# Kernel tuning notes

Hardware: AMD Instinct MI355X
Metric: run time of the kernel (lower is better)

The kernel has to match this reference:

```python
import jax, jax.numpy as jnp
import numpy as np

B, C, L = 8, 512, 4096
KC, VC, H = 512, 512, 8
DK, DV = KC // H, VC // H
EPS = 1e-5


def _ln(x, g, b):
    m = jnp.mean(x, axis=-1, keepdims=True)
    v = jnp.var(x, axis=-1, keepdims=True)
    return (x - m) * jax.lax.rsqrt(v + EPS) * g + b


def setup_inputs() -> dict:
    key = jax.random.key(0)
    ks = jax.random.split(key, 12)
    s = 0.02
    return {
        "z1": jax.random.normal(ks[0], (B, C, L), jnp.float32),
        "z2": jax.random.normal(ks[1], (B, C, L), jnp.float32),
        "Wq": jax.random.normal(ks[2], (KC, C), jnp.float32) * s,
        "bq": jnp.zeros((KC,), jnp.float32),
        "Wk": jax.random.normal(ks[3], (KC, C), jnp.float32) * s,
        "bk": jnp.zeros((KC,), jnp.float32),
        "Wv": jax.random.normal(ks[4], (VC, C), jnp.float32) * s,
        "bv": jnp.zeros((VC,), jnp.float32),
        "Wr": jax.random.normal(ks[5], (C, VC), jnp.float32) * s,
        "br": jnp.zeros((C,), jnp.float32),
        "g1": jnp.ones((C,), jnp.float32),
        "be1": jnp.zeros((C,), jnp.float32),
        "W1": jax.random.normal(ks[6], (2 * C, C), jnp.float32) * s,
        "b1": jnp.zeros((2 * C,), jnp.float32),
        "W2": jax.random.normal(ks[7], (C, 2 * C), jnp.float32) * s,
        "b2": jnp.zeros((C,), jnp.float32),
        "g2": jnp.ones((C,), jnp.float32),
        "be2": jnp.zeros((C,), jnp.float32),
    }


def reference(z1, z2, Wq, bq, Wk, bk, Wv, bv, Wr, br, g1, be1, W1, b1, W2, b2, g2, be2):
    # 1x1 Conv1d projections (channels-first)
    q = jnp.einsum('oc,bcl->bol', Wq, z1) + bq[None, :, None]
    k = jnp.einsum('oc,bcl->bol', Wk, z2) + bk[None, :, None]
    v = jnp.einsum('oc,bcl->bol', Wv, z2) + bv[None, :, None]
    qh = q.reshape(B, H, DK, L)
    kh = k.reshape(B, H, DK, L)
    vh = v.reshape(B, H, DV, L)
    # efficient attention: keys softmax over length, queries over channels
    kh = jax.nn.softmax(kh, axis=-1)
    qh = jax.nn.softmax(qh, axis=2)
    ctx = jnp.einsum('bhkl,bhvl->bhkv', kh, vh)          # [B,H,DK,DV]
    att = jnp.einsum('bhkv,bhkl->bhvl', ctx, qh)          # [B,H,DV,L]
    att = att.reshape(B, VC, L)
    z = jnp.einsum('oc,bcl->bol', Wr, att) + br[None, :, None] + z1  # reprojection + residual
    # b c l -> b l c, LayerNorm, FFN, back
    x = z.transpose(0, 2, 1)
    x = _ln(x, g1, be1)
    h = jax.nn.elu(x @ W1.T + b1)
    y = h @ W2.T + b2
    y = _ln(y, g2, be2)
    return y.transpose(0, 2, 1)
```

## Files before the change

kernel.cpp:

```cpp
#include <hip/hip_runtime.h>
#include <math.h>

#define B_   8
#define C_   512
#define L_   4096
#define H_   8
#define DK_  64
#define C2_  1024

typedef unsigned short ushort;
typedef short     bf16x8_t __attribute__((ext_vector_type(8)));
typedef float     f32x4_t  __attribute__((ext_vector_type(4)));
typedef unsigned short u16x8 __attribute__((ext_vector_type(8)));
typedef unsigned short u16x4 __attribute__((ext_vector_type(4)));

__device__ __forceinline__ float bf2f(ushort u) {
    unsigned int x = ((unsigned int)u) << 16;
    float f; __builtin_memcpy(&f, &x, 4); return f;
}
__device__ __forceinline__ ushort f2bf(float f) {
    unsigned int x; __builtin_memcpy(&x, &f, 4);
    x = (x + 0x7FFFu + ((x >> 16) & 1u)) >> 16;
    return (ushort)x;
}

#define GLOAD_LDS16(gp, lp) \
    __builtin_amdgcn_global_load_lds((const __attribute__((address_space(1))) void*)(gp), \
                                     (__attribute__((address_space(3))) void*)(lp), 16, 0, 0)

__global__ __launch_bounds__(256) void transpose_in(const float* __restrict__ in,
                                                    ushort* __restrict__ out)
{
    const int b = blockIdx.z, c0 = blockIdx.y * 64, l0 = blockIdx.x * 64;
    __shared__ float t[64][65];
    const int tid = threadIdx.x;
    {
        const int c = tid >> 4, l4 = (tid & 15) * 4;
        const float* ip = in + ((size_t)b * C_ + c0) * L_ + l0;
#pragma unroll
        for (int cc = c; cc < 64; cc += 16) {
            float4 v = *(const float4*)(ip + (size_t)cc * L_ + l4);
            t[l4 + 0][cc] = v.x; t[l4 + 1][cc] = v.y;
            t[l4 + 2][cc] = v.z; t[l4 + 3][cc] = v.w;
        }
    }
    __syncthreads();
    {
        const int l = tid >> 3, c8 = (tid & 7) * 8;
        ushort* op = out + ((size_t)b * L_ + l0) * C_ + c0;
#pragma unroll
        for (int ll = l; ll < 64; ll += 32) {
            u16x8 v;
#pragma unroll
            for (int i = 0; i < 8; ++i) v[i] = f2bf(t[ll][c8 + i]);
            *(u16x8*)(op + (size_t)ll * C_ + c8) = v;
        }
    }
}

__global__ __launch_bounds__(256) void transpose_out(const float* __restrict__ in,
                                                     float* __restrict__ out)
{
    const int b = blockIdx.z, c0 = blockIdx.y * 64, l0 = blockIdx.x * 64;
    __shared__ float t[64][65];
    const int tid = threadIdx.x;
    {
        const int l = tid >> 4, c4 = (tid & 15) * 4;
#pragma unroll
        for (int ll = l; ll < 64; ll += 16) {
            float4 v = *(const float4*)(in + ((size_t)(b * L_ + l0 + ll)) * C_ + c0 + c4);
            t[c4 + 0][ll] = v.x; t[c4 + 1][ll] = v.y;
            t[c4 + 2][ll] = v.z; t[c4 + 3][ll] = v.w;
        }
    }
    __syncthreads();
    {
        const int c = tid >> 4, l4 = (tid & 15) * 4;
        float* op = out + ((size_t)b * C_ + c0) * L_ + l0;
#pragma unroll
        for (int cc = c; cc < 64; cc += 16) {
            float4 v = {t[cc][l4], t[cc][l4 + 1], t[cc][l4 + 2], t[cc][l4 + 3]};
            *(float4*)(op + (size_t)cc * L_ + l4) = v;
        }
    }
}

__global__ __launch_bounds__(256) void cvt_bf16(const float* __restrict__ in,
                                                ushort* __restrict__ out, int n4)
{
    const int i = blockIdx.x * 256 + threadIdx.x;
    if (i < n4) {
        float4 v = *(const float4*)(in + 4 * (size_t)i);
        u16x4 o; o[0] = f2bf(v.x); o[1] = f2bf(v.y); o[2] = f2bf(v.z); o[3] = f2bf(v.w);
        *(u16x4*)(out + 4 * (size_t)i) = o;
    }
}

__global__ __launch_bounds__(256) void zero_kernel(float* __restrict__ p, int n4)
{
    const int i = blockIdx.x * 256 + threadIdx.x;
    if (i < n4) { float4 z = {0.f, 0.f, 0.f, 0.f}; *(float4*)(p + 4 * (size_t)i) = z; }
}

template<int ACT, bool HAS_RES>
__global__ __launch_bounds__(512, 2) void conv_mfma(
    const ushort* __restrict__ A, const ushort* __restrict__ Wt,
    const float* __restrict__ bias, const ushort* __restrict__ res,
    ushort* __restrict__ out, int M, int N, int K)
{
    const int m0 = blockIdx.x * 256;
    const int n0 = blockIdx.y * 256;
    const int tid = threadIdx.x;
    const int w = tid >> 6, lane = tid & 63;
    const int wm2 = (w >> 2) * 128, wn = (w & 3) * 64;
    const int l16 = lane & 15, quad = lane >> 4;

    __shared__ ushort smem[65536];

    const int sRow = tid >> 1, sHalf = tid & 1;
    const int sh = sHalf ^ ((sRow >> 2) & 1);
    const ushort* gA = A  + (size_t)(m0 + sRow) * K + sh * 8;
    const ushort* gB = Wt + (size_t)(n0 + sRow) * K + sh * 8;
    const int ldst = tid * 8;

    const int baseA = wm2 + l16;
    const int baseB = wn + l16;
    const int hA = (quad & 1) ^ ((baseA >> 2) & 1);
    const int hB = (quad & 1) ^ ((baseB >> 2) & 1);
    const int qhi = (quad >> 1) * 4096;
    const int aoff = qhi + baseA * 16 + hA * 8;
    const int boff = qhi + 16384 + baseB * 16 + hB * 8;

    f32x4_t acc[8][4];
#pragma unroll
    for (int i = 0; i < 8; ++i)
#pragma unroll
        for (int j = 0; j < 4; ++j) acc[i][j] = (f32x4_t){0.f, 0.f, 0.f, 0.f};

    const int nt = K >> 6;

#pragma unroll
    for (int q = 0; q < 4; ++q) {
        GLOAD_LDS16(gA + q * 16, smem + q * 4096 + ldst);
        GLOAD_LDS16(gB + q * 16, smem + 16384 + q * 4096 + ldst);
    }

    for (int t = 0; t < nt; ++t) {
        const int cb = (t & 1) * 32768;
        const int nb = 32768 - cb;
        const bool pf = (t + 1 < nt);
#pragma unroll
        for (int p = 0; p < 4; ++p) {
            if (pf) {
                const int ko = (t + 1) * 64 + p * 16;
                GLOAD_LDS16(gA + ko, smem + nb + p * 4096 + ldst);
                GLOAD_LDS16(gB + ko, smem + nb + 16384 + p * 4096 + ldst);
                asm volatile("s_waitcnt vmcnt(6)" ::: "memory");
            } else {
                if (p < 2) { asm volatile("s_waitcnt vmcnt(4)" ::: "memory"); }
                else       { asm volatile("s_waitcnt vmcnt(0)" ::: "memory"); }
            }
            __builtin_amdgcn_s_barrier();
            asm volatile("" ::: "memory");

            const int ih = p & 1;
            const ushort* base = smem + cb + (p >> 1) * 8192;
            bf16x8_t wf[4], af[4];
#pragma unroll
            for (int x = 0; x < 4; ++x) {
                wf[x] = *(const bf16x8_t*)(base + boff + x * 256);
                af[x] = *(const bf16x8_t*)(base + aoff + (ih * 4 + x) * 256);
            }
            __builtin_amdgcn_s_setprio(1);
#pragma unroll
            for (int x = 0; x < 4; ++x)
#pragma unroll
                for (int j = 0; j < 4; ++j)
                    acc[ih * 4 + x][j] =
                        __builtin_amdgcn_mfma_f32_16x16x32_bf16(wf[j], af[x], acc[ih * 4 + x][j], 0, 0, 0);
            __builtin_amdgcn_s_setprio(0);
        }
    }

    __syncthreads();
    ushort* sT = smem + w * 4608;
#pragma unroll
    for (int h2 = 0; h2 < 2; ++h2) {
#pragma unroll
        for (int j = 0; j < 4; ++j) {
            const int nb4 = wn + j * 16 + quad * 4;
            const float4 bo = *(const float4*)(bias + n0 + nb4);
            const float bv[4] = {bo.x, bo.y, bo.z, bo.w};
#pragma unroll
            for (int x = 0; x < 4; ++x) {
                const int ml = x * 16 + l16;
                const int m = m0 + wm2 + h2 * 64 + ml;
                float v[4];
#pragma unroll
                for (int r = 0; r < 4; ++r) v[r] = acc[h2 * 4 + x][j][r] + bv[r];
                if (HAS_RES) {
                    const u16x4 rv = *(const u16x4*)(res + (size_t)m * N + n0 + nb4);
#pragma unroll
                    for (int r = 0; r < 4; ++r) v[r] += bf2f(rv[r]);
                }
                if (ACT == 1) {
#pragma unroll
                    for (int r = 0; r < 4; ++r) v[r] = (v[r] > 0.f) ? v[r] : (__expf(v[r]) - 1.f);
                }
                u16x4 pv;
#pragma unroll
                for (int r = 0; r < 4; ++r) pv[r] = f2bf(v[r]);
                *(u16x4*)(sT + ml * 72 + (nb4 - wn)) = pv;
            }
        }
        {
            const int rr = lane >> 3, ch = lane & 7;
#pragma unroll
            for (int rep = 0; rep < 8; ++rep) {
                const int ml = rep * 8 + rr;
                const u16x8 vo = *(const u16x8*)(sT + ml * 72 + ch * 8);
                *(u16x8*)(out + (size_t)(m0 + wm2 + h2 * 64 + ml) * N + n0 + wn + ch * 8) = vo;
            }
        }
    }
}

__global__ __launch_bounds__(256) void kstat_chunk(const ushort* __restrict__ k,
                                                   float2* __restrict__ stats)
{
    const int cg = blockIdx.x;
    const int bc = blockIdx.y;
    const int b = bc >> 3, ch = bc & 7;
    const int tid = threadIdx.x;
    const int g = tid & 7;
    const int kk = tid >> 3;
    const int w = tid >> 6, lane = tid & 63;
    const ushort* base = k + ((size_t)(b * L_) + ch * 512) * C_ + cg * 64 + g * 8;

    __shared__ float red[4][8][8];
    __shared__ float mcol[64];

    float fm[8];
#pragma unroll
    for (int i = 0; i < 8; ++i) fm[i] = -3.0e38f;
    for (int r = kk; r < 512; r += 32) {
        u16x8 v = *(const u16x8*)(base + (size_t)r * C_);
#pragma unroll
        for (int i = 0; i < 8; ++i) fm[i] = fmaxf(fm[i], bf2f(v[i]));
    }
#pragma unroll
    for (int off = 8; off <= 32; off <<= 1)
#pragma unroll
        for (int i = 0; i < 8; ++i) fm[i] = fmaxf(fm[i], __shfl_xor(fm[i], off));
    if ((lane >> 3) == 0)
#pragma unroll
        for (int i = 0; i < 8; ++i) red[w][g][i] = fm[i];
    __syncthreads();
    if (tid < 64) {
        const int g2 = tid >> 3, j = tid & 7;
        mcol[g2 * 8 + j] = fmaxf(fmaxf(red[0][g2][j], red[1][g2][j]),
                                 fmaxf(red[2][g2][j], red[3][g2][j]));
    }
    __syncthreads();
    float fmc[8];
#pragma unroll
    for (int i = 0; i < 8; ++i) fmc[i] = mcol[g * 8 + i];

    float fs[8] = {};
    for (int r = kk; r < 512; r += 32) {
        u16x8 v = *(const u16x8*)(base + (size_t)r * C_);
#pragma unroll
        for (int i = 0; i < 8; ++i) fs[i] += __expf(bf2f(v[i]) - fmc[i]);
    }
#pragma unroll
    for (int off = 8; off <= 32; off <<= 1)
#pragma unroll
        for (int i = 0; i < 8; ++i) fs[i] += __shfl_xor(fs[i], off);
    __syncthreads();
    if ((lane >> 3) == 0)
#pragma unroll
        for (int i = 0; i < 8; ++i) red[w][g][i] = fs[i];
    __syncthreads();
    if (tid < 64) {
        const int g2 = tid >> 3, j = tid & 7;
        const float s = red[0][g2][j] + red[1][g2][j] + red[2][g2][j] + red[3][g2][j];
        const int c = cg * 64 + g2 * 8 + j;
        stats[((size_t)(b * C_ + c)) * 8 + ch] = make_float2(mcol[g2 * 8 + j], s);
    }
}

__global__ __launch_bounds__(256) void kstat_merge(const float2* __restrict__ stats,
                                                   float2* __restrict__ minv)
{
    const int i = blockIdx.x * 256 + threadIdx.x;
    if (i >= B_ * C_) return;
    float2 st[8];
    float m = -3.0e38f;
#pragma unroll
    for (int ch = 0; ch < 8; ++ch) { st[ch] = stats[(size_t)i * 8 + ch]; m = fmaxf(m, st[ch].x); }
    float s = 0.f;
#pragma unroll
    for (int ch = 0; ch < 8; ++ch) s += st[ch].y * __expf(st[ch].x - m);
    minv[i] = make_float2(m, 1.f / s);
}

__global__ __launch_bounds__(256) void ctx_mfma(
    const ushort* __restrict__ kk, const ushort* __restrict__ vv,
    const float2* __restrict__ minv, float* __restrict__ ctx)
{
    const int bh = blockIdx.y, b = bh >> 3, h = bh & 7;
    const int l0 = blockIdx.x * 256;
    const int tid = threadIdx.x, w = tid >> 6, lane = tid & 63;
    const int l16 = lane & 15, quad = lane >> 4;

    __shared__ ushort sK[64 * 72];
    __shared__ ushort sV[64 * 72];

    const int grp = tid >> 7;
    const int st  = tid & 127;
    const int sc8 = (st & 7) * 8;
    const int sl4 = (st >> 3) * 4;
    const ushort* gsrc = (grp ? vv : kk)
        + ((size_t)(b * L_ + l0 + sl4)) * C_ + h * 64 + sc8;
    ushort* dst = grp ? sV : sK;

    float2 cst[8];
#pragma unroll
    for (int i = 0; i < 8; ++i)
        cst[i] = minv[(size_t)b * C_ + h * 64 + sc8 + i];

    f32x4_t acc[4];
#pragma unroll
    for (int j = 0; j < 4; ++j) acc[j] = (f32x4_t){0.f, 0.f, 0.f, 0.f};

    for (int tile = 0; tile < 4; ++tile) {
        u16x8 vr[4];
#pragma unroll
        for (int j = 0; j < 4; ++j)
            vr[j] = *(const u16x8*)(gsrc + ((size_t)(tile * 64 + j)) * C_);
        __syncthreads();
        if (grp == 0) {
#pragma unroll
            for (int c = 0; c < 8; ++c) {
                u16x4 o;
#pragma unroll
                for (int j = 0; j < 4; ++j)
                    o[j] = f2bf(__expf(bf2f(vr[j][c]) - cst[c].x) * cst[c].y);
                *(u16x4*)(dst + (sc8 + c) * 72 + sl4) = o;
            }
        } else {
#pragma unroll
            for (int c = 0; c < 8; ++c) {
                u16x4 o;
#pragma unroll
                for (int j = 0; j < 4; ++j) o[j] = vr[j][c];
                *(u16x4*)(dst + (sc8 + c) * 72 + sl4) = o;
            }
        }
        __syncthreads();
#pragma unroll
        for (int k0 = 0; k0 < 64; k0 += 32) {
            const bf16x8_t vf = *(const bf16x8_t*)(sV + (w * 16 + l16) * 72 + k0 + quad * 8);
#pragma unroll
            for (int j = 0; j < 4; ++j) {
                const bf16x8_t kf = *(const bf16x8_t*)(sK + (j * 16 + l16) * 72 + k0 + quad * 8);
                acc[j] = __builtin_amdgcn_mfma_f32_16x16x32_bf16(vf, kf, acc[j], 0, 0, 0);
            }
        }
    }
    float* cp = ctx + (size_t)bh * 4096;
#pragma unroll
    for (int j = 0; j < 4; ++j)
#pragma unroll
        for (int r = 0; r < 4; ++r)
            atomicAdd(&cp[(w * 16 + quad * 4 + r) * 64 + (j * 16 + l16)], acc[j][r]);
}

__global__ __launch_bounds__(256) void att_mfma(
    const ushort* __restrict__ q, const float* __restrict__ ctx,
    ushort* __restrict__ att)
{
    const int bh = blockIdx.y, b = bh >> 3, h = bh & 7;
    const int l0 = blockIdx.x * 128;
    const int tid = threadIdx.x, w = tid >> 6, lane = tid & 63;
    const int l16 = lane & 15, quad = lane >> 4;

    __shared__ ushort sQ[128 * 72];
    __shared__ ushort sC[64 * 72];

    {
        const int part = tid & 7;
#pragma unroll
        for (int rr = tid >> 3; rr < 128; rr += 32) {
            u16x8 v = *(const u16x8*)(q + ((size_t)(b * L_ + l0 + rr)) * C_ + h * 64 + part * 8);
            float f[8], m = -3.0e38f;
#pragma unroll
            for (int i = 0; i < 8; ++i) { f[i] = bf2f(v[i]); m = fmaxf(m, f[i]); }
            m = fmaxf(m, __shfl_xor(m, 1));
            m = fmaxf(m, __shfl_xor(m, 2));
            m = fmaxf(m, __shfl_xor(m, 4));
            float s = 0.f;
#pragma unroll
            for (int i = 0; i < 8; ++i) { f[i] = __expf(f[i] - m); s += f[i]; }
            s += __shfl_xor(s, 1); s += __shfl_xor(s, 2); s += __shfl_xor(s, 4);
            const float inv = 1.f / s;
            u16x8 o;
#pragma unroll
            for (int i = 0; i < 8; ++i) o[i] = f2bf(f[i] * inv);
            *(u16x8*)(sQ + rr * 72 + part * 8) = o;
        }
        const int dv = tid >> 2, dk0 = (tid & 3) * 16;
        const float* cp = ctx + (size_t)bh * 4096 + dv * 64 + dk0;
#pragma unroll
        for (int i = 0; i < 16; ++i) sC[dv * 72 + dk0 + i] = f2bf(cp[i]);
    }
    __syncthreads();

    f32x4_t acc[2][4];
#pragma unroll
    for (int i = 0; i < 2; ++i)
#pragma unroll
        for (int j = 0; j < 4; ++j) acc[i][j] = (f32x4_t){0.f, 0.f, 0.f, 0.f};

#pragma unroll
    for (int ks = 0; ks < 2; ++ks) {
        const int k0 = ks * 32;
        bf16x8_t aq[2], bc[4];
#pragma unroll
        for (int i = 0; i < 2; ++i)
            aq[i] = *(const bf16x8_t*)(sQ + (w * 32 + i * 16 + l16) * 72 + k0 + quad * 8);
#pragma unroll
        for (int j = 0; j < 4; ++j)
            bc[j] = *(const bf16x8_t*)(sC + (j * 16 + l16) * 72 + k0 + quad * 8);
#pragma unroll
        for (int i = 0; i < 2; ++i)
#pragma unroll
            for (int j = 0; j < 4; ++j)
                acc[i][j] = __builtin_amdgcn_mfma_f32_16x16x32_bf16(aq[i], bc[j], acc[i][j], 0, 0, 0);
    }

#pragma unroll
    for (int j = 0; j < 4; ++j)
#pragma unroll
        for (int i = 0; i < 2; ++i) {
            const int mb = l0 + w * 32 + i * 16 + quad * 4;
#pragma unroll
            for (int r = 0; r < 4; ++r)
                att[((size_t)(b * L_ + mb + r)) * C_ + h * 64 + j * 16 + l16] = f2bf(acc[i][j][r]);
        }
}

template<bool OUTF32>
__global__ __launch_bounds__(256) void ln_row(
    const ushort* __restrict__ in, const float* __restrict__ g,
    const float* __restrict__ be, ushort* __restrict__ outb,
    float* __restrict__ outf)
{
    const int tid = threadIdx.x, w = tid >> 6, lane = tid & 63;
    const size_t row = (size_t)blockIdx.x * 4 + w;
    const ushort* p = in + row * C_ + lane * 8;
    u16x8 v = *(const u16x8*)p;
    float f[8], s = 0.f, s2 = 0.f;
#pragma unroll
    for (int i = 0; i < 8; ++i) { f[i] = bf2f(v[i]); s += f[i]; s2 = fmaf(f[i], f[i], s2); }
#pragma unroll
    for (int o = 1; o < 64; o <<= 1) { s += __shfl_xor(s, o); s2 += __shfl_xor(s2, o); }
    const float mean = s * (1.f / C_);
    const float var  = s2 * (1.f / C_) - mean * mean;
    const float inv  = rsqrtf(var + 1e-5f);
    if (OUTF32) {
        float* op = outf + row * C_ + lane * 8;
#pragma unroll
        for (int i = 0; i < 8; ++i)
            op[i] = (f[i] - mean) * inv * g[lane * 8 + i] + be[lane * 8 + i];
    } else {
        u16x8 ov;
#pragma unroll
        for (int i = 0; i < 8; ++i)
            ov[i] = f2bf((f[i] - mean) * inv * g[lane * 8 + i] + be[lane * 8 + i]);
        *(u16x8*)(outb + row * C_ + lane * 8) = ov;
    }
}

extern "C" void kernel_launch(void* const* d_in, const int* in_sizes, int n_in,
                              void* d_out, int out_size, void* d_ws, size_t ws_size,
                              hipStream_t stream)
{
    const float* z1  = (const float*)d_in[0];
    const float* z2  = (const float*)d_in[1];
    const float* Wq  = (const float*)d_in[2];
    const float* bq  = (const float*)d_in[3];
    const float* Wk  = (const float*)d_in[4];
    const float* bk  = (const float*)d_in[5];
    const float* Wv  = (const float*)d_in[6];
    const float* bv  = (const float*)d_in[7];
    const float* Wr  = (const float*)d_in[8];
    const float* br  = (const float*)d_in[9];
    const float* g1  = (const float*)d_in[10];
    const float* be1 = (const float*)d_in[11];
    const float* W1  = (const float*)d_in[12];
    const float* b1  = (const float*)d_in[13];
    const float* W2  = (const float*)d_in[14];
    const float* b2  = (const float*)d_in[15];
    const float* g2  = (const float*)d_in[16];
    const float* be2 = (const float*)d_in[17];
    float* out = (float*)d_out;

    const size_t SB = (size_t)B_ * L_ * C_;
    ushort* ws16 = (ushort*)d_ws;
    ushort* b0v = ws16;
    ushort* b1v = ws16 + SB;
    ushort* b2v = ws16 + 2 * SB;
    ushort* b3v = ws16 + 3 * SB;
    ushort* wb  = ws16 + 4 * SB;
    ushort* wbq = wb;
    ushort* wbk = wb + 262144;
    ushort* wbv = wb + 524288;
    ushort* wbr = wb + 786432;
    ushort* wb1 = wb + 1048576;
    ushort* wb2 = wb + 1572864;
    float*  ctxf = (float*)(wb + 2097152);
    float2* stats = (float2*)(ctxf + 65536);
    float2* minv  = stats + (size_t)B_ * C_ * 8;
    ushort* vbuf = (ushort*)d_out;
    ushort* hbuf = (ushort*)d_out;
    float*  yf32 = (float*)b2v;

    const dim3 blk(256);
    const dim3 blk512(512);
    const int M = B_ * L_;

    transpose_in<<<dim3(L_/64, C_/64, B_), blk, 0, stream>>>(z1, b0v);
    transpose_in<<<dim3(L_/64, C_/64, B_), blk, 0, stream>>>(z2, b1v);
    cvt_bf16<<<dim3(262144/4/256), blk, 0, stream>>>(Wq, wbq, 262144/4);
    cvt_bf16<<<dim3(262144/4/256), blk, 0, stream>>>(Wk, wbk, 262144/4);
    cvt_bf16<<<dim3(262144/4/256), blk, 0, stream>>>(Wv, wbv, 262144/4);
    cvt_bf16<<<dim3(262144/4/256), blk, 0, stream>>>(Wr, wbr, 262144/4);
    cvt_bf16<<<dim3(524288/4/256), blk, 0, stream>>>(W1, wb1, 524288/4);
    cvt_bf16<<<dim3(524288/4/256), blk, 0, stream>>>(W2, wb2, 524288/4);

    conv_mfma<0,false><<<dim3(M/256, C_/256), blk512, 0, stream>>>(b0v, wbq, bq, nullptr, b2v, M, C_, C_);
    conv_mfma<0,false><<<dim3(M/256, C_/256), blk512, 0, stream>>>(b1v, wbk, bk, nullptr, b3v, M, C_, C_);
    conv_mfma<0,false><<<dim3(M/256, C_/256), blk512, 0, stream>>>(b1v, wbv, bv, nullptr, vbuf, M, C_, C_);

    kstat_chunk<<<dim3(C_/64, B_ * 8), blk, 0, stream>>>(b3v, stats);
    kstat_merge<<<dim3((B_ * C_ + 255) / 256), blk, 0, stream>>>(stats, minv);

    zero_kernel<<<dim3(65536/256), blk, 0, stream>>>(ctxf, 65536);
    ctx_mfma<<<dim3(16, B_ * H_), blk, 0, stream>>>(b3v, vbuf, minv, ctxf);

    att_mfma<<<dim3(L_/128, B_ * H_), blk, 0, stream>>>(b2v, ctxf, b1v);

    conv_mfma<0,true><<<dim3(M/256, C_/256), blk512, 0, stream>>>(b1v, wbr, br, b0v, b2v, M, C_, C_);

    ln_row<false><<<dim3(M/4), blk, 0, stream>>>(b2v, g1, be1, b3v, nullptr);

    conv_mfma<1,false><<<dim3(M/256, C2_/256), blk512, 0, stream>>>(b3v, wb1, b1, nullptr, hbuf, M, C2_, C_);

    conv_mfma<0,false><<<dim3(M/256, C_/256), blk512, 0, stream>>>(hbuf, wb2, b2, nullptr, b0v, M, C_, C2_);

    ln_row<true><<<dim3(M/4), blk, 0, stream>>>(b0v, g2, be2, nullptr, yf32);

    transpose_out<<<dim3(L_/64, C_/64, B_), blk, 0, stream>>>(yf32, out);
}
```

Before: 519.5 us.

## Restructure conv GEMM main loop with row-major swizzled LDS and staged prefetch

Rewrites the bf16 MFMA GEMM inner loop to use a row-major 64-wide LDS tile with an XOR swizzle, loading operands per 16-row group. Global-to-LDS prefetch for the next K tile is split into four half-tile stages, each interleaved between MFMA phases and fenced by barriers and sched_barriers. Launch bounds drop to one block per SM to allow more registers. The aim is to overlap memory traffic with MFMA work and cut LDS bank conflicts. The cost is lower occupancy and many more barriers per iteration, and the removed final __syncthreads before the epilogue reuses LDS, which could race.

```diff
diff --git a/kernel.cpp b/kernel.cpp
--- a/kernel.cpp
+++ b/kernel.cpp
@@ -103,7 +103,7 @@
 }
 
 template<int ACT, bool HAS_RES>
-__global__ __launch_bounds__(512, 2) void conv_mfma(
+__global__ __launch_bounds__(512, 1) void conv_mfma(
     const ushort* __restrict__ A, const ushort* __restrict__ Wt,
     const float* __restrict__ bias, const ushort* __restrict__ res,
     ushort* __restrict__ out, int M, int N, int K)
@@ -112,24 +112,36 @@
     const int n0 = blockIdx.y * 256;
     const int tid = threadIdx.x;
     const int w = tid >> 6, lane = tid & 63;
-    const int wm2 = (w >> 2) * 128, wn = (w & 3) * 64;
+    const int wmh = w >> 2;
+    const int wn = (w & 3) * 64;
+    const int bhalf = (w & 3) >> 1;
+    const int brow0 = (w & 1) * 64;
     const int l16 = lane & 15, quad = lane >> 4;
 
     __shared__ ushort smem[65536];
 
-    const int sRow = tid >> 1, sHalf = tid & 1;
-    const int sh = sHalf ^ ((sRow >> 2) & 1);
-    const ushort* gA = A  + (size_t)(m0 + sRow) * K + sh * 8;
-    const ushort* gB = Wt + (size_t)(n0 + sRow) * K + sh * 8;
-    const int ldst = tid * 8;
-
-    const int baseA = wm2 + l16;
-    const int baseB = wn + l16;
-    const int hA = (quad & 1) ^ ((baseA >> 2) & 1);
-    const int hB = (quad & 1) ^ ((baseB >> 2) & 1);
-    const int qhi = (quad >> 1) * 4096;
-    const int aoff = qhi + baseA * 16 + hA * 8;
-    const int boff = qhi + 16384 + baseB * 16 + hB * 8;
+    const int rl = tid >> 3;
+    const int sp = (tid & 7) ^ ((rl & 1) << 2) ^ (((rl >> 2) & 1) << 1);
+    const ushort* gA[4]; const ushort* gB[4];
+#pragma unroll
+    for (int r4 = 0; r4 < 4; ++r4) {
+        gA[r4] = A  + (size_t)(m0 + r4 * 64 + rl) * K + sp * 8;
+        gB[r4] = Wt + (size_t)(n0 + r4 * 64 + rl) * K + sp * 8;
+    }
+#define STAGE_A(h, kt, nbuf) do { \
+        ushort* l0 = smem + (nbuf) + (h) * 8192 + tid * 8; \
+        GLOAD_LDS16(gA[(h)*2]     + (size_t)(kt) * 64, l0); \
+        GLOAD_LDS16(gA[(h)*2 + 1] + (size_t)(kt) * 64, l0 + 4096); \
+    } while (0)
+#define STAGE_B(h, kt, nbuf) do { \
+        ushort* l0 = smem + (nbuf) + 16384 + (h) * 8192 + tid * 8; \
+        GLOAD_LDS16(gB[(h)*2]     + (size_t)(kt) * 64, l0); \
+        GLOAD_LDS16(gB[(h)*2 + 1] + (size_t)(kt) * 64, l0 + 4096); \
+    } while (0)
+
+    const int fl  = ((l16 & 1) << 2) | (((l16 >> 2) & 1) << 1);
+    const int sx0 = (0 * 4 + quad) ^ fl;
+    const int sx1 = (1 * 4 + quad) ^ fl;
 
     f32x4_t acc[8][4];
 #pragma unroll
@@ -139,50 +151,88 @@
 
     const int nt = K >> 6;
 
-#pragma unroll
-    for (int q = 0; q < 4; ++q) {
-        GLOAD_LDS16(gA + q * 16, smem + q * 4096 + ldst);
-        GLOAD_LDS16(gB + q * 16, smem + 16384 + q * 4096 + ldst);
-    }
-
-    for (int t = 0; t < nt; ++t) {
-        const int cb = (t & 1) * 32768;
+    STAGE_A(0, 0, 0); STAGE_A(1, 0, 0); STAGE_B(0, 0, 0); STAGE_B(1, 0, 0);
+
+    for (int T = 0; T < nt; ++T) {
+        const int cb = (T & 1) * 32768;
         const int nb = 32768 - cb;
-        const bool pf = (t + 1 < nt);
-#pragma unroll
-        for (int p = 0; p < 4; ++p) {
-            if (pf) {
-                const int ko = (t + 1) * 64 + p * 16;
-                GLOAD_LDS16(gA + ko, smem + nb + p * 4096 + ldst);
-                GLOAD_LDS16(gB + ko, smem + nb + 16384 + p * 4096 + ldst);
-                asm volatile("s_waitcnt vmcnt(6)" ::: "memory");
-            } else {
-                if (p < 2) { asm volatile("s_waitcnt vmcnt(4)" ::: "memory"); }
-                else       { asm volatile("s_waitcnt vmcnt(0)" ::: "memory"); }
-            }
-            __builtin_amdgcn_s_barrier();
-            asm volatile("" ::: "memory");
-
-            const int ih = p & 1;
-            const ushort* base = smem + cb + (p >> 1) * 8192;
-            bf16x8_t wf[4], af[4];
-#pragma unroll
-            for (int x = 0; x < 4; ++x) {
-                wf[x] = *(const bf16x8_t*)(base + boff + x * 256);
-                af[x] = *(const bf16x8_t*)(base + aoff + (ih * 4 + x) * 256);
-            }
-            __builtin_amdgcn_s_setprio(1);
-#pragma unroll
-            for (int x = 0; x < 4; ++x)
-#pragma unroll
-                for (int j = 0; j < 4; ++j)
-                    acc[ih * 4 + x][j] =
-                        __builtin_amdgcn_mfma_f32_16x16x32_bf16(wf[j], af[x], acc[ih * 4 + x][j], 0, 0, 0);
-            __builtin_amdgcn_s_setprio(0);
-        }
-    }
-
-    __syncthreads();
+        const bool pf = (T + 1 < nt);
+        const ushort* aB = smem + cb + wmh * 8192;
+        const ushort* bB = smem + cb + 16384 + bhalf * 8192 + brow0 * 64;
+        bf16x8_t bfr[4], af[4];
+
+        if (pf) STAGE_A(0, T + 1, nb);
+        __builtin_amdgcn_sched_barrier(0);
+        if (pf) { asm volatile("s_waitcnt vmcnt(2)" ::: "memory"); }
+        else    { asm volatile("s_waitcnt vmcnt(0)" ::: "memory"); }
+        __builtin_amdgcn_s_barrier();
+        __builtin_amdgcn_sched_barrier(0);
+#pragma unroll
+        for (int j = 0; j < 4; ++j)
+            bfr[j] = *(const bf16x8_t*)(bB + (j * 16 + l16) * 64 + sx0 * 8);
+#pragma unroll
+        for (int x = 0; x < 4; ++x)
+            af[x] = *(const bf16x8_t*)(aB + (x * 16 + l16) * 64 + sx0 * 8);
+        __builtin_amdgcn_s_setprio(1);
+#pragma unroll
+        for (int x = 0; x < 4; ++x)
+#pragma unroll
+            for (int j = 0; j < 4; ++j)
+                acc[x][j] = __builtin_amdgcn_mfma_f32_16x16x32_bf16(bfr[j], af[x], acc[x][j], 0, 0, 0);
+        __builtin_amdgcn_s_setprio(0);
+        __builtin_amdgcn_s_barrier();
+
+#pragma unroll
+        for (int x = 0; x < 4; ++x)
+            af[x] = *(const bf16x8_t*)(aB + ((x + 4) * 16 + l16) * 64 + sx0 * 8);
+        if (pf) STAGE_A(1, T + 1, nb);
+        __builtin_amdgcn_s_barrier();
+        __builtin_amdgcn_sched_barrier(0);
+        __builtin_amdgcn_s_setprio(1);
+#pragma unroll
+        for (int x = 0; x < 4; ++x)
+#pragma unroll
+            for (int j = 0; j < 4; ++j)
+                acc[x + 4][j] = __builtin_amdgcn_mfma_f32_16x16x32_bf16(bfr[j], af[x], acc[x + 4][j], 0, 0, 0);
+        __builtin_amdgcn_s_setprio(0);
+        __builtin_amdgcn_s_barrier();
+
+#pragma unroll
+        for (int j = 0; j < 4; ++j)
+            bfr[j] = *(const bf16x8_t*)(bB + (j * 16 + l16) * 64 + sx1 * 8);
+#pragma unroll
+        for (int x = 0; x < 4; ++x)
+            af[x] = *(const bf16x8_t*)(aB + (x * 16 + l16) * 64 + sx1 * 8);
+        if (pf) STAGE_B(0, T + 1, nb);
+        __builtin_amdgcn_s_barrier();
+        __builtin_amdgcn_sched_barrier(0);
+        __builtin_amdgcn_s_setprio(1);
+#pragma unroll
+        for (int x = 0; x < 4; ++x)
+#pragma unroll
+            for (int j = 0; j < 4; ++j)
+                acc[x][j] = __builtin_amdgcn_mfma_f32_16x16x32_bf16(bfr[j], af[x], acc[x][j], 0, 0, 0);
+        __builtin_amdgcn_s_setprio(0);
+        __builtin_amdgcn_s_barrier();
+
+#pragma unroll
+        for (int x = 0; x < 4; ++x)
+            af[x] = *(const bf16x8_t*)(aB + ((x + 4) * 16 + l16) * 64 + sx1 * 8);
+        if (pf) STAGE_B(1, T + 1, nb);
+        __builtin_amdgcn_s_barrier();
+        __builtin_amdgcn_sched_barrier(0);
+        __builtin_amdgcn_s_setprio(1);
+#pragma unroll
+        for (int x = 0; x < 4; ++x)
+#pragma unroll
+            for (int j = 0; j < 4; ++j)
+                acc[x + 4][j] = __builtin_amdgcn_mfma_f32_16x16x32_bf16(bfr[j], af[x], acc[x + 4][j], 0, 0, 0);
+        __builtin_amdgcn_s_setprio(0);
+        __builtin_amdgcn_s_barrier();
+    }
+#undef STAGE_A
+#undef STAGE_B
+
     ushort* sT = smem + w * 4608;
 #pragma unroll
     for (int h2 = 0; h2 < 2; ++h2) {
@@ -194,7 +244,7 @@
 #pragma unroll
             for (int x = 0; x < 4; ++x) {
                 const int ml = x * 16 + l16;
-                const int m = m0 + wm2 + h2 * 64 + ml;
+                const int m = m0 + wmh * 128 + h2 * 64 + ml;
                 float v[4];
 #pragma unroll
                 for (int r = 0; r < 4; ++r) v[r] = acc[h2 * 4 + x][j][r] + bv[r];
@@ -219,7 +269,7 @@
             for (int rep = 0; rep < 8; ++rep) {
                 const int ml = rep * 8 + rr;
                 const u16x8 vo = *(const u16x8*)(sT + ml * 72 + ch * 8);
-                *(u16x8*)(out + (size_t)(m0 + wm2 + h2 * 64 + ml) * N + n0 + wn + ch * 8) = vo;
+                *(u16x8*)(out + (size_t)(m0 + wmh * 128 + h2 * 64 + ml) * N + n0 + wn + ch * 8) = vo;
             }
         }
     }
```

New measurement: 502.5 us. 1.03x faster.
